# Optimization experiments

Measured on AMD Instinct MI355X. Metric: run time of the kernel, lower is better.

Reference implementation:

```python
import jax, jax.numpy as jnp
import numpy as np

TOKENS, D_IN, D_OUT = 16384, 4096, 4096


def setup_inputs() -> dict:
    key = jax.random.key(0)
    kx, kw, kb = jax.random.split(key, 3)
    x = jax.random.normal(kx, (TOKENS, D_IN), dtype=jnp.float32)
    W = jax.random.normal(kw, (D_OUT, D_IN), dtype=jnp.float32) * 0.02
    b = jax.random.normal(kb, (D_OUT,), dtype=jnp.float32) * 0.02
    return {"x": x, "W": W, "b": b}


def reference(x, W, b):
    # mean-abs scale computed from the full-precision input
    x_mean = jnp.mean(jnp.abs(x))
    # binarize activations and weights via sign(), run the wrapped Linear
    y = jnp.sign(x) @ jnp.sign(W).T + b  # [TOKENS, D_OUT]
    # rescale output by the activation scale
    return y * x_mean
```

## Files before the change

### kernel.cpp

```cpp
#include <hip/hip_runtime.h>
#include <stdint.h>

#define TOKENS 16384
#define D_IN   4096
#define D_OUT  4096
#define NKT    32

typedef int   v4i  __attribute__((ext_vector_type(4)));
typedef int   v8i  __attribute__((ext_vector_type(8)));
typedef float v16f __attribute__((ext_vector_type(16)));

__device__ __forceinline__ void gl_lds16(const void* g, void* l) {
    __builtin_amdgcn_global_load_lds(
        (const __attribute__((address_space(1))) void*)g,
        (__attribute__((address_space(3))) void*)l, 16, 0, 0);
}

#define BARRIER() __builtin_amdgcn_s_barrier()

__device__ __forceinline__ unsigned fp4c(float f) {
    return (f > 0.f) ? 0x2u : ((f < 0.f) ? 0xAu : 0u);
}


__global__ __launch_bounds__(256) void pack_x_abssum(
        const float* __restrict__ x, unsigned char* __restrict__ xp,
        float* __restrict__ partials) {
    __shared__ unsigned short tile16[128 * 33];
    __shared__ float wsum[4];
    const int b  = blockIdx.x;
    const int mb = b >> 5;
    const int KT = b & 31;
    const int t  = threadIdx.x;
    const float* src = x + (size_t)mb * 128 * D_IN + KT * 128;
    float accum = 0.f;
#pragma unroll
    for (int p = 0; p < 16; ++p) {
        const int idx = p * 256 + t;
        const int r   = idx >> 5;
        const int c4  = idx & 31;
        float4 v = *(const float4*)(src + (size_t)r * D_IN + c4 * 4);
        tile16[r * 33 + c4] = (unsigned short)(fp4c(v.x) | (fp4c(v.y) << 4)
                             | (fp4c(v.z) << 8) | (fp4c(v.w) << 12));
        accum += fabsf(v.x) + fabsf(v.y) + fabsf(v.z) + fabsf(v.w);
    }
    __syncthreads();
    unsigned* dst = (unsigned*)(xp + ((size_t)mb * 32 + KT) * 8192);
#pragma unroll
    for (int w = 0; w < 8; ++w) {
        const int i    = w * 256 + t;
        const int c    = i >> 2;
        const int j2   = (i & 3) * 4;
        const int uks  = c >> 6;
        const int lane = c & 63;
        const int row  = (uks >> 1) * 32 + (lane & 31);
        const int c4a  = (uks & 1) * 16 + (lane >> 5) * 8 + (j2 >> 1);
        dst[i] = (unsigned)tile16[row * 33 + c4a]
               | ((unsigned)tile16[row * 33 + c4a + 1] << 16);
    }
#pragma unroll
    for (int o = 32; o > 0; o >>= 1) accum += __shfl_down(accum, o);
    if ((t & 63) == 0) wsum[t >> 6] = accum;
    __syncthreads();
    if (t == 0) partials[b] = wsum[0] + wsum[1] + wsum[2] + wsum[3];
}

__global__ void reduce_partials(const float* __restrict__ p, float* __restrict__ s) {
    __shared__ float ws[4];
    float a = 0.f;
    for (int i = threadIdx.x; i < 4096; i += 256) a += p[i];
#pragma unroll
    for (int o = 32; o > 0; o >>= 1) a += __shfl_down(a, o);
    if ((threadIdx.x & 63) == 0) ws[threadIdx.x >> 6] = a;
    __syncthreads();
    if (threadIdx.x == 0) s[0] = ws[0] + ws[1] + ws[2] + ws[3];
}

__global__ __launch_bounds__(256) void pack_w_kernel(
        const float* __restrict__ wsrc, unsigned char* __restrict__ wp) {
    __shared__ unsigned short tile16[256 * 33];
    const int b  = blockIdx.x;
    const int nb = b >> 5;
    const int KT = b & 31;
    const int t  = threadIdx.x;
    const float* src = wsrc + (size_t)nb * 256 * D_IN + KT * 128;
#pragma unroll
    for (int p = 0; p < 32; ++p) {
        const int idx = p * 256 + t;
        const int r   = idx >> 5;
        const int c4  = idx & 31;
        float4 v = *(const float4*)(src + (size_t)r * D_IN + c4 * 4);
        tile16[r * 33 + c4] = (unsigned short)(fp4c(v.x) | (fp4c(v.y) << 4)
                             | (fp4c(v.z) << 8) | (fp4c(v.w) << 12));
    }
    __syncthreads();
    unsigned* dst = (unsigned*)(wp + ((size_t)nb * 32 + KT) * 16384);
#pragma unroll
    for (int w = 0; w < 16; ++w) {
        const int i    = w * 256 + t;
        const int c    = i >> 2;
        const int j2   = (i & 3) * 4;
        const int uks  = c >> 6;
        const int lane = c & 63;
        const int row  = (uks >> 1) * 32 + (lane & 31);
        const int c4a  = (uks & 1) * 16 + (lane >> 5) * 8 + (j2 >> 1);
        dst[i] = (unsigned)tile16[row * 33 + c4a]
               | ((unsigned)tile16[row * 33 + c4a + 1] << 16);
    }
}


#define STAGE(d, kt) do {                                               \
    signed char* L_ = (signed char*)&ldsA[d][0];                        \
    const signed char* ga_ = aG + (size_t)(kt) * 8192;                  \
    const signed char* gb_ = bG + (size_t)(kt) * 16384;                 \
    gl_lds16(ga_ + t16,         L_ + t16);                              \
    gl_lds16(ga_ + 4096 + t16,  L_ + 4096 + t16);                      \
    gl_lds16(gb_ + t16,         L_ + 8192 + t16);                      \
    gl_lds16(gb_ + 4096 + t16,  L_ + 12288 + t16);                     \
    gl_lds16(gb_ + 8192 + t16,  L_ + 16384 + t16);                     \
    gl_lds16(gb_ + 12288 + t16, L_ + 20480 + t16);                     \
} while (0)

#define READ_KS0(dst, bufv) do {                                        \
    const v4i* L_ = &ldsA[bufv][0];                                     \
    dst[0] = L_[auo + lane];            dst[1] = L_[auo + 128 + lane];  \
    dst[2] = L_[buo + lane];            dst[3] = L_[buo + 128 + lane];  \
    dst[4] = L_[buo + 256 + lane];      dst[5] = L_[buo + 384 + lane];  \
} while (0)

#define READ_KS1(dst, bufv) do {                                        \
    const v4i* L_ = &ldsA[bufv][0];                                     \
    dst[0] = L_[auo + 64 + lane];       dst[1] = L_[auo + 192 + lane];  \
    dst[2] = L_[buo + 64 + lane];       dst[3] = L_[buo + 192 + lane];  \
    dst[4] = L_[buo + 320 + lane];      dst[5] = L_[buo + 448 + lane];  \
} while (0)

__device__ __forceinline__ v8i dup8(v4i v) {
    return __builtin_shufflevector(v, v, 0, 1, 2, 3, 0, 1, 2, 3);
}

#define MFMA4(d, a, b) __builtin_amdgcn_mfma_scale_f32_32x32x64_f8f6f4( \
    (a), (b), (d), 4, 4, 0, 0x7F7F7F7F, 0, 0x7F7F7F7F)

#define CLUSTER(F) do {                                                 \
    _Pragma("unroll")                                                   \
    for (int an = 0; an < 4; ++an) {                                    \
        acc[0][an] = MFMA4(acc[0][an], dup8(F[0]), dup8(F[2 + an]));    \
        acc[1][an] = MFMA4(acc[1][an], dup8(F[1]), dup8(F[2 + an]));    \
    }                                                                   \
} while (0)

__global__ __launch_bounds__(256, 2) void bin_gemm(
    const unsigned char* __restrict__ Ap, const unsigned char* __restrict__ Bp,
    const float* __restrict__ bias, const float* __restrict__ sum_ptr,
    float* __restrict__ out) {
    __shared__ v4i ldsA[3][1536];

    const int t    = threadIdx.x;
    const int t16  = t * 16;
    const int lane = t & 63;
    const int wid  = t >> 6;
    const int wm   = wid >> 1;
    const int wn   = wid & 1;
    const int auo  = (wm * 2) * 128;
    const int buo  = 512 + (wn * 4) * 128;

    const int bid   = blockIdx.x;
    const int xcd   = bid & 7;
    const int local = bid >> 3;
    const int nb    = xcd * 2 + (local & 1);
    const int mb    = local >> 1;

    const signed char* aG = (const signed char*)Ap + (size_t)mb * 32 * 8192;
    const signed char* bG = (const signed char*)Bp + (size_t)nb * 32 * 16384;

    v16f acc[2][4];
#pragma unroll
    for (int i = 0; i < 2; ++i)
#pragma unroll
        for (int j = 0; j < 4; ++j) acc[i][j] = (v16f)(0.f);

    v4i P[6], Q[6];

    STAGE(0, 0);
    STAGE(1, 1);
    asm volatile("s_waitcnt vmcnt(6)" ::: "memory");
    BARRIER();
    READ_KS0(P, 0);
    READ_KS1(Q, 0);

    int cb = 0, rb = 1, sb = 2;
    for (int kt = 0; kt < NKT - 1; ++kt) {
        CLUSTER(P);
        if (kt < NKT - 2) STAGE(sb, kt + 2);
        asm volatile("s_waitcnt lgkmcnt(0)" ::: "memory");
        if (kt == NKT - 2) { asm volatile("s_waitcnt vmcnt(0)" ::: "memory"); }
        else               { asm volatile("s_waitcnt vmcnt(6)" ::: "memory"); }
        BARRIER();
        READ_KS0(P, rb);
        CLUSTER(Q);
        READ_KS1(Q, rb);
        const int n0 = rb, n1 = sb, n2 = cb;
        cb = n0; rb = n1; sb = n2;
    }
    CLUSTER(P);
    CLUSTER(Q);

    const float scale = *sum_ptr * (1.0f / 67108864.0f);
    const int rbase = mb * 128 + wm * 64 + 4 * (lane >> 5);
    const int cbase = nb * 256 + wn * 128 + (lane & 31);
#pragma unroll
    for (int an = 0; an < 4; ++an) {
        const int col = cbase + an * 32;
        const float bb = bias[col];
#pragma unroll
        for (int am = 0; am < 2; ++am) {
            const int r0 = rbase + am * 32;
#pragma unroll
            for (int g = 0; g < 16; ++g) {
                const int row = r0 + (g & 3) + 8 * (g >> 2);
                out[(size_t)row * D_OUT + col] =
                    (acc[am][an][g] + bb) * scale;
            }
        }
    }
}

extern "C" void kernel_launch(void* const* d_in, const int* in_sizes, int n_in,
                              void* d_out, int out_size, void* d_ws, size_t ws_size,
                              hipStream_t stream) {
    const float* x = (const float*)d_in[0];
    const float* W = (const float*)d_in[1];
    const float* b = (const float*)d_in[2];
    float* out = (float*)d_out;

    float* sum_ptr    = (float*)d_ws;
    float* partials   = (float*)d_ws + 64;
    unsigned char* xs = (unsigned char*)d_ws + 65536;
    unsigned char* wp = xs + (size_t)128 * 32 * 8192;

    pack_x_abssum<<<128 * 32, 256, 0, stream>>>(x, xs, partials);
    reduce_partials<<<1, 256, 0, stream>>>(partials, sum_ptr);
    pack_w_kernel<<<16 * 32, 256, 0, stream>>>(W, wp);
    bin_gemm<<<2048, 256, 0, stream>>>(xs, wp, b, sum_ptr, out);
}
```

Baseline: 226.5 us.

## Enlarge binary GEMM block tile to 256x256 with 512-thread workgroups

The GEMM block tile grows from 128x256 to 256x256, served by 8 waves each computing a 128x64 sub-tile. The activation packing kernel is changed to emit 256-row packed blocks to match. LDS staging buffers grow accordingly, and the partial-sum reduction and launch grids are resized. The aim is more reuse of each staged A/B tile and less global and L2 traffic per MFMA. In exchange, the triple-buffered LDS footprint grows and each block runs alone on a CU.

```diff
diff --git a/kernel.cpp b/kernel.cpp
--- a/kernel.cpp
+++ b/kernel.cpp
@@ -26,16 +26,16 @@
 __global__ __launch_bounds__(256) void pack_x_abssum(
         const float* __restrict__ x, unsigned char* __restrict__ xp,
         float* __restrict__ partials) {
-    __shared__ unsigned short tile16[128 * 33];
+    __shared__ unsigned short tile16[256 * 33];
     __shared__ float wsum[4];
     const int b  = blockIdx.x;
     const int mb = b >> 5;
     const int KT = b & 31;
     const int t  = threadIdx.x;
-    const float* src = x + (size_t)mb * 128 * D_IN + KT * 128;
+    const float* src = x + (size_t)mb * 256 * D_IN + KT * 128;
     float accum = 0.f;
 #pragma unroll
-    for (int p = 0; p < 16; ++p) {
+    for (int p = 0; p < 32; ++p) {
         const int idx = p * 256 + t;
         const int r   = idx >> 5;
         const int c4  = idx & 31;
@@ -45,56 +45,7 @@
         accum += fabsf(v.x) + fabsf(v.y) + fabsf(v.z) + fabsf(v.w);
     }
     __syncthreads();
-    unsigned* dst = (unsigned*)(xp + ((size_t)mb * 32 + KT) * 8192);
-#pragma unroll
-    for (int w = 0; w < 8; ++w) {
-        const int i    = w * 256 + t;
-        const int c    = i >> 2;
-        const int j2   = (i & 3) * 4;
-        const int uks  = c >> 6;
-        const int lane = c & 63;
-        const int row  = (uks >> 1) * 32 + (lane & 31);
-        const int c4a  = (uks & 1) * 16 + (lane >> 5) * 8 + (j2 >> 1);
-        dst[i] = (unsigned)tile16[row * 33 + c4a]
-               | ((unsigned)tile16[row * 33 + c4a + 1] << 16);
-    }
-#pragma unroll
-    for (int o = 32; o > 0; o >>= 1) accum += __shfl_down(accum, o);
-    if ((t & 63) == 0) wsum[t >> 6] = accum;
-    __syncthreads();
-    if (t == 0) partials[b] = wsum[0] + wsum[1] + wsum[2] + wsum[3];
-}
-
-__global__ void reduce_partials(const float* __restrict__ p, float* __restrict__ s) {
-    __shared__ float ws[4];
-    float a = 0.f;
-    for (int i = threadIdx.x; i < 4096; i += 256) a += p[i];
-#pragma unroll
-    for (int o = 32; o > 0; o >>= 1) a += __shfl_down(a, o);
-    if ((threadIdx.x & 63) == 0) ws[threadIdx.x >> 6] = a;
-    __syncthreads();
-    if (threadIdx.x == 0) s[0] = ws[0] + ws[1] + ws[2] + ws[3];
-}
-
-__global__ __launch_bounds__(256) void pack_w_kernel(
-        const float* __restrict__ wsrc, unsigned char* __restrict__ wp) {
-    __shared__ unsigned short tile16[256 * 33];
-    const int b  = blockIdx.x;
-    const int nb = b >> 5;
-    const int KT = b & 31;
-    const int t  = threadIdx.x;
-    const float* src = wsrc + (size_t)nb * 256 * D_IN + KT * 128;
-#pragma unroll
-    for (int p = 0; p < 32; ++p) {
-        const int idx = p * 256 + t;
-        const int r   = idx >> 5;
-        const int c4  = idx & 31;
-        float4 v = *(const float4*)(src + (size_t)r * D_IN + c4 * 4);
-        tile16[r * 33 + c4] = (unsigned short)(fp4c(v.x) | (fp4c(v.y) << 4)
-                             | (fp4c(v.z) << 8) | (fp4c(v.w) << 12));
-    }
-    __syncthreads();
-    unsigned* dst = (unsigned*)(wp + ((size_t)nb * 32 + KT) * 16384);
+    unsigned* dst = (unsigned*)(xp + ((size_t)mb * 32 + KT) * 16384);
 #pragma unroll
     for (int w = 0; w < 16; ++w) {
         const int i    = w * 256 + t;
@@ -107,33 +58,76 @@
         dst[i] = (unsigned)tile16[row * 33 + c4a]
                | ((unsigned)tile16[row * 33 + c4a + 1] << 16);
     }
+#pragma unroll
+    for (int o = 32; o > 0; o >>= 1) accum += __shfl_down(accum, o);
+    if ((t & 63) == 0) wsum[t >> 6] = accum;
+    __syncthreads();
+    if (t == 0) partials[b] = wsum[0] + wsum[1] + wsum[2] + wsum[3];
+}
+
+__global__ void reduce_partials(const float* __restrict__ p, float* __restrict__ s) {
+    __shared__ float ws[4];
+    float a = 0.f;
+    for (int i = threadIdx.x; i < 2048; i += 256) a += p[i];
+#pragma unroll
+    for (int o = 32; o > 0; o >>= 1) a += __shfl_down(a, o);
+    if ((threadIdx.x & 63) == 0) ws[threadIdx.x >> 6] = a;
+    __syncthreads();
+    if (threadIdx.x == 0) s[0] = ws[0] + ws[1] + ws[2] + ws[3];
+}
+
+__global__ __launch_bounds__(256) void pack_w_kernel(
+        const float* __restrict__ wsrc, unsigned char* __restrict__ wp) {
+    __shared__ unsigned short tile16[256 * 33];
+    const int b  = blockIdx.x;
+    const int nb = b >> 5;
+    const int KT = b & 31;
+    const int t  = threadIdx.x;
+    const float* src = wsrc + (size_t)nb * 256 * D_IN + KT * 128;
+#pragma unroll
+    for (int p = 0; p < 32; ++p) {
+        const int idx = p * 256 + t;
+        const int r   = idx >> 5;
+        const int c4  = idx & 31;
+        float4 v = *(const float4*)(src + (size_t)r * D_IN + c4 * 4);
+        tile16[r * 33 + c4] = (unsigned short)(fp4c(v.x) | (fp4c(v.y) << 4)
+                             | (fp4c(v.z) << 8) | (fp4c(v.w) << 12));
+    }
+    __syncthreads();
+    unsigned* dst = (unsigned*)(wp + ((size_t)nb * 32 + KT) * 16384);
+#pragma unroll
+    for (int w = 0; w < 16; ++w) {
+        const int i    = w * 256 + t;
+        const int c    = i >> 2;
+        const int j2   = (i & 3) * 4;
+        const int uks  = c >> 6;
+        const int lane = c & 63;
+        const int row  = (uks >> 1) * 32 + (lane & 31);
+        const int c4a  = (uks & 1) * 16 + (lane >> 5) * 8 + (j2 >> 1);
+        dst[i] = (unsigned)tile16[row * 33 + c4a]
+               | ((unsigned)tile16[row * 33 + c4a + 1] << 16);
+    }
 }
 
 
 #define STAGE(d, kt) do {                                               \
-    signed char* L_ = (signed char*)&ldsA[d][0];                        \
-    const signed char* ga_ = aG + (size_t)(kt) * 8192;                  \
+    signed char* L_ = (signed char*)&ldsT[d][0];                        \
+    const signed char* ga_ = aG + (size_t)(kt) * 16384;                 \
     const signed char* gb_ = bG + (size_t)(kt) * 16384;                 \
-    gl_lds16(ga_ + t16,         L_ + t16);                              \
-    gl_lds16(ga_ + 4096 + t16,  L_ + 4096 + t16);                      \
-    gl_lds16(gb_ + t16,         L_ + 8192 + t16);                      \
-    gl_lds16(gb_ + 4096 + t16,  L_ + 12288 + t16);                     \
-    gl_lds16(gb_ + 8192 + t16,  L_ + 16384 + t16);                     \
-    gl_lds16(gb_ + 12288 + t16, L_ + 20480 + t16);                     \
+    gl_lds16(ga_ + t16,        L_ + t16);                               \
+    gl_lds16(ga_ + 8192 + t16, L_ + 8192 + t16);                       \
+    gl_lds16(gb_ + t16,        L_ + 16384 + t16);                      \
+    gl_lds16(gb_ + 8192 + t16, L_ + 24576 + t16);                      \
 } while (0)
 
-#define READ_KS0(dst, bufv) do {                                        \
-    const v4i* L_ = &ldsA[bufv][0];                                     \
-    dst[0] = L_[auo + lane];            dst[1] = L_[auo + 128 + lane];  \
-    dst[2] = L_[buo + lane];            dst[3] = L_[buo + 128 + lane];  \
-    dst[4] = L_[buo + 256 + lane];      dst[5] = L_[buo + 384 + lane];  \
-} while (0)
-
-#define READ_KS1(dst, bufv) do {                                        \
-    const v4i* L_ = &ldsA[bufv][0];                                     \
-    dst[0] = L_[auo + 64 + lane];       dst[1] = L_[auo + 192 + lane];  \
-    dst[2] = L_[buo + 64 + lane];       dst[3] = L_[buo + 192 + lane];  \
-    dst[4] = L_[buo + 320 + lane];      dst[5] = L_[buo + 448 + lane];  \
+#define READ_KS(dst, bufv, ks) do {                                     \
+    const v4i* L_ = &ldsT[bufv][0];                                     \
+    dst[0] = L_[auo + (ks) * 64 + lane];                                \
+    dst[1] = L_[auo + 128 + (ks) * 64 + lane];                          \
+    dst[2] = L_[auo + 256 + (ks) * 64 + lane];                          \
+    dst[3] = L_[auo + 384 + (ks) * 64 + lane];                          \
+    dst[4] = L_[buo + (ks) * 64 + lane];                                \
+    dst[5] = L_[buo + 128 + (ks) * 64 + lane];                          \
 } while (0)
 
 __device__ __forceinline__ v8i dup8(v4i v) {
@@ -145,26 +139,26 @@
 
 #define CLUSTER(F) do {                                                 \
     _Pragma("unroll")                                                   \
-    for (int an = 0; an < 4; ++an) {                                    \
-        acc[0][an] = MFMA4(acc[0][an], dup8(F[0]), dup8(F[2 + an]));    \
-        acc[1][an] = MFMA4(acc[1][an], dup8(F[1]), dup8(F[2 + an]));    \
+    for (int am = 0; am < 4; ++am) {                                    \
+        acc[am][0] = MFMA4(acc[am][0], dup8(F[am]), dup8(F[4]));        \
+        acc[am][1] = MFMA4(acc[am][1], dup8(F[am]), dup8(F[5]));        \
     }                                                                   \
 } while (0)
 
-__global__ __launch_bounds__(256, 2) void bin_gemm(
+__global__ __launch_bounds__(512, 1) void bin_gemm(
     const unsigned char* __restrict__ Ap, const unsigned char* __restrict__ Bp,
     const float* __restrict__ bias, const float* __restrict__ sum_ptr,
     float* __restrict__ out) {
-    __shared__ v4i ldsA[3][1536];
+    __shared__ v4i ldsT[3][2048];
 
     const int t    = threadIdx.x;
     const int t16  = t * 16;
     const int lane = t & 63;
     const int wid  = t >> 6;
-    const int wm   = wid >> 1;
-    const int wn   = wid & 1;
-    const int auo  = (wm * 2) * 128;
-    const int buo  = 512 + (wn * 4) * 128;
+    const int wm   = wid >> 2;
+    const int wn   = wid & 3;
+    const int auo  = (wm * 4) * 128;
+    const int buo  = 1024 + (wn * 2) * 128;
 
     const int bid   = blockIdx.x;
     const int xcd   = bid & 7;
@@ -172,23 +166,23 @@
     const int nb    = xcd * 2 + (local & 1);
     const int mb    = local >> 1;
 
-    const signed char* aG = (const signed char*)Ap + (size_t)mb * 32 * 8192;
+    const signed char* aG = (const signed char*)Ap + (size_t)mb * 32 * 16384;
     const signed char* bG = (const signed char*)Bp + (size_t)nb * 32 * 16384;
 
-    v16f acc[2][4];
-#pragma unroll
-    for (int i = 0; i < 2; ++i)
-#pragma unroll
-        for (int j = 0; j < 4; ++j) acc[i][j] = (v16f)(0.f);
+    v16f acc[4][2];
+#pragma unroll
+    for (int i = 0; i < 4; ++i)
+#pragma unroll
+        for (int j = 0; j < 2; ++j) acc[i][j] = (v16f)(0.f);
 
     v4i P[6], Q[6];
 
     STAGE(0, 0);
     STAGE(1, 1);
-    asm volatile("s_waitcnt vmcnt(6)" ::: "memory");
+    asm volatile("s_waitcnt vmcnt(4)" ::: "memory");
     BARRIER();
-    READ_KS0(P, 0);
-    READ_KS1(Q, 0);
+    READ_KS(P, 0, 0);
+    READ_KS(Q, 0, 1);
 
     int cb = 0, rb = 1, sb = 2;
     for (int kt = 0; kt < NKT - 1; ++kt) {
@@ -196,11 +190,11 @@
         if (kt < NKT - 2) STAGE(sb, kt + 2);
         asm volatile("s_waitcnt lgkmcnt(0)" ::: "memory");
         if (kt == NKT - 2) { asm volatile("s_waitcnt vmcnt(0)" ::: "memory"); }
-        else               { asm volatile("s_waitcnt vmcnt(6)" ::: "memory"); }
+        else               { asm volatile("s_waitcnt vmcnt(4)" ::: "memory"); }
         BARRIER();
-        READ_KS0(P, rb);
+        READ_KS(P, rb, 0);
         CLUSTER(Q);
-        READ_KS1(Q, rb);
+        READ_KS(Q, rb, 1);
         const int n0 = rb, n1 = sb, n2 = cb;
         cb = n0; rb = n1; sb = n2;
     }
@@ -208,14 +202,14 @@
     CLUSTER(Q);
 
     const float scale = *sum_ptr * (1.0f / 67108864.0f);
-    const int rbase = mb * 128 + wm * 64 + 4 * (lane >> 5);
-    const int cbase = nb * 256 + wn * 128 + (lane & 31);
-#pragma unroll
-    for (int an = 0; an < 4; ++an) {
+    const int rbase = mb * 256 + wm * 128 + 4 * (lane >> 5);
+    const int cbase = nb * 256 + wn * 64 + (lane & 31);
+#pragma unroll
+    for (int an = 0; an < 2; ++an) {
         const int col = cbase + an * 32;
         const float bb = bias[col];
 #pragma unroll
-        for (int am = 0; am < 2; ++am) {
+        for (int am = 0; am < 4; ++am) {
             const int r0 = rbase + am * 32;
 #pragma unroll
             for (int g = 0; g < 16; ++g) {
@@ -238,10 +232,10 @@
     float* sum_ptr    = (float*)d_ws;
     float* partials   = (float*)d_ws + 64;
     unsigned char* xs = (unsigned char*)d_ws + 65536;
-    unsigned char* wp = xs + (size_t)128 * 32 * 8192;
-
-    pack_x_abssum<<<128 * 32, 256, 0, stream>>>(x, xs, partials);
+    unsigned char* wp = xs + (size_t)64 * 32 * 16384;
+
+    pack_x_abssum<<<64 * 32, 256, 0, stream>>>(x, xs, partials);
     reduce_partials<<<1, 256, 0, stream>>>(partials, sum_ptr);
     pack_w_kernel<<<16 * 32, 256, 0, stream>>>(W, wp);
-    bin_gemm<<<2048, 256, 0, stream>>>(xs, wp, b, sum_ptr, out);
-}
+    bin_gemm<<<1024, 512, 0, stream>>>(xs, wp, b, sum_ptr, out);
+}
```

Measured after the change: 228.0 us. About the same (+0.7%).
